# Kernel tuning notes

Hardware: AMD Instinct MI355X
Metric: run time of the kernel (lower is better)

Reference implementation:

```python
import jax, jax.numpy as jnp
import numpy as np

B, T = 32, 256
DM, DL, DH, DP, E = 256, 256, 512, 16, 8


def setup_inputs() -> dict:
    key = jax.random.key(0)
    ks = jax.random.split(key, 20)
    s = 0.02
    d = {
        "z": jax.random.normal(ks[0], (B, T, DL), jnp.float32),
        "p_next": jax.random.normal(ks[1], (B, T, DP), jnp.float32),
        "v_hip_next": jax.random.normal(ks[2], (B, T, 3), jnp.float32),
        "x_curr": jax.random.normal(ks[3], (B, T, DM), jnp.float32),
        # gating: Linear(DL+DP->DH), Linear(DL+DH->DH), Linear(DL+DH->E)
        "gw0": jax.random.normal(ks[4], (DL + DP, DH), jnp.float32) * s,
        "gb0": jnp.zeros((DH,), jnp.float32),
        "gw1": jax.random.normal(ks[5], (DL + DH, DH), jnp.float32) * s,
        "gb1": jnp.zeros((DH,), jnp.float32),
        "gw2": jax.random.normal(ks[6], (DL + DH, E), jnp.float32) * s,
        "gb2": jnp.zeros((E,), jnp.float32),
        # expert (MultiLinear) weights: (E, d_in, d_out)
        "w0": jax.random.normal(ks[7], (E, DM + 3 + DL, DH), jnp.float32) * s,
        "b0": jnp.zeros((E, DH), jnp.float32),
        "w1": jax.random.normal(ks[8], (E, DH + DL, DH), jnp.float32) * s,
        "b1": jnp.zeros((E, DH), jnp.float32),
        "w2": jax.random.normal(ks[9], (E, DH + DL, DH), jnp.float32) * s,
        "b2": jnp.zeros((E, DH), jnp.float32),
        "wo": jax.random.normal(ks[10], (E, DH + DL, DM), jnp.float32) * s,
        "bo": jnp.zeros((E, DM), jnp.float32),
    }
    return d


def _gating(z, p, gw0, gb0, gw1, gb1, gw2, gb2):
    h = jax.nn.elu(jnp.concatenate([z, p], axis=-1) @ gw0 + gb0)
    h = jax.nn.elu(jnp.concatenate([z, h], axis=-1) @ gw1 + gb1)
    h = jax.nn.softmax(jnp.concatenate([z, h], axis=-1) @ gw2 + gb2, axis=-1)
    return h  # (B, T, E)


def _moe_layer(x, w, b, ew):
    # x: (B,T,Din), w: (E,Din,Dout), b: (E,Dout), ew: (B,T,E)
    y = jnp.einsum('btd,edh->bteh', x, w) + b  # (B,T,E,Dout)
    return jnp.sum(y * ew[..., None], axis=-2)  # (B,T,Dout)


def reference(z, p_next, v_hip_next, x_curr,
              gw0, gb0, gw1, gb1, gw2, gb2,
              w0, b0, w1, b1, w2, b2, wo, bo):
    ew = _gating(z, p_next, gw0, gb0, gw1, gb1, gw2, gb2)
    x = jnp.concatenate([v_hip_next, x_curr], axis=-1)
    for w, b in ((w0, b0), (w1, b1), (w2, b2)):
        x = jnp.concatenate([z, x], axis=-1)
        x = jax.nn.elu(_moe_layer(x, w, b, ew))
    x = jnp.concatenate([z, x], axis=-1)
    return _moe_layer(x, wo, bo, ew)  # (B,T,DM)
```

## Files before the change

kernel.cpp:

```cpp
#include <hip/hip_runtime.h>
#include <cstdint>
#include <cstddef>

using u16 = unsigned short;
using bf16x8 = __attribute__((ext_vector_type(8))) __bf16;
using f32x4  = __attribute__((ext_vector_type(4))) float;

static __device__ __forceinline__ u16 f2bf(float f) {
  unsigned u = __builtin_bit_cast(unsigned, f);
  unsigned r = (u + 0x7fffu + ((u >> 16) & 1u)) >> 16;
  return (u16)r;
}
static __device__ __forceinline__ float bf2f(u16 h) {
  unsigned u = ((unsigned)h) << 16;
  return __builtin_bit_cast(float, u);
}
static __device__ __forceinline__ float eluf(float x) {
  return x > 0.f ? x : expm1f(x);
}
static __device__ __forceinline__ void gload16(const u16* g, u16* l) {
  __builtin_amdgcn_global_load_lds(
      (const __attribute__((address_space(1))) void*)g,
      (__attribute__((address_space(3))) void*)l, 16, 0, 0);
}

__global__ void transpose_convert(const float* __restrict__ src, u16* __restrict__ dst,
                                  int Ksrc, int Nsrc, int Kpad, int E) {
  __shared__ float tile[32][33];
  const int e  = blockIdx.z;
  const int k0 = blockIdx.x * 32;
  const int d0 = blockIdx.y * 32;
  const int tx = threadIdx.x;
  const int ty = threadIdx.y;
  const float* s = src + (size_t)e * Ksrc * Nsrc;
#pragma unroll
  for (int i = 0; i < 4; ++i) {
    const int k = k0 + ty + i * 8;
    float v = 0.f;
    if (k < Ksrc) v = s[(size_t)k * Nsrc + d0 + tx];
    tile[ty + i * 8][tx] = v;
  }
  __syncthreads();
#pragma unroll
  for (int i = 0; i < 4; ++i) {
    const int d = d0 + ty + i * 8;
    dst[((size_t)d * E + e) * Kpad + k0 + tx] = f2bf(tile[tx][ty + i * 8]);
  }
}

__global__ void prep_cat(const float* __restrict__ z, const float* __restrict__ p,
                         const float* __restrict__ vh, const float* __restrict__ xc,
                         u16* __restrict__ catP, u16* __restrict__ catE0,
                         u16* __restrict__ cat0, u16* __restrict__ cat1) {
  const int m = blockIdx.x;
  const int t = threadIdx.x;
  const u16 zb = f2bf(z[(size_t)m * 256 + t]);
  catP [(size_t)m * 288 + t] = zb;
  catE0[(size_t)m * 576 + t] = zb;
  cat0 [(size_t)m * 768 + t] = zb;
  cat1 [(size_t)m * 768 + t] = zb;
  if (t < 32) {
    const u16 val = (t < 16) ? f2bf(p[(size_t)m * 16 + t]) : (u16)0;
    catP[(size_t)m * 288 + 256 + t] = val;
  }
  for (int c = 256 + t; c < 576; c += 256) {
    const int idx = c - 256;
    float v = 0.f;
    if (idx < 3)        v = vh[(size_t)m * 3 + idx];
    else if (idx < 259) v = xc[(size_t)m * 256 + (idx - 3)];
    catE0[(size_t)m * 576 + c] = f2bf(v);
  }
}

__global__ __launch_bounds__(256) void gating_tail(const u16* __restrict__ cat,
                                                   const float* __restrict__ gw2,
                                                   const float* __restrict__ gb2,
                                                   float* __restrict__ ew) {
  const int ln = threadIdx.x & 63;
  const int token = (int)((blockIdx.x * 256 + threadIdx.x) >> 6);
  const u16* row = cat + (size_t)token * 768;
  float a[8] = {0.f, 0.f, 0.f, 0.f, 0.f, 0.f, 0.f, 0.f};
#pragma unroll
  for (int kk = 0; kk < 12; ++kk) {
    const int k = kk * 64 + ln;
    const float x = bf2f(row[k]);
    const float4* wr = reinterpret_cast<const float4*>(gw2 + (size_t)k * 8);
    const float4 w0 = wr[0], w1 = wr[1];
    a[0] += x * w0.x; a[1] += x * w0.y; a[2] += x * w0.z; a[3] += x * w0.w;
    a[4] += x * w1.x; a[5] += x * w1.y; a[6] += x * w1.z; a[7] += x * w1.w;
  }
#pragma unroll
  for (int j = 0; j < 8; ++j) {
#pragma unroll
    for (int d = 32; d > 0; d >>= 1) a[j] += __shfl_xor(a[j], d);
    a[j] += gb2[j];
  }
  float mx = a[0];
#pragma unroll
  for (int j = 1; j < 8; ++j) mx = fmaxf(mx, a[j]);
  float s = 0.f, pj[8];
#pragma unroll
  for (int j = 0; j < 8; ++j) { pj[j] = expf(a[j] - mx); s += pj[j]; }
  const float inv = 1.f / s;
  if (ln == 0) {
#pragma unroll
    for (int j = 0; j < 8; ++j) ew[(size_t)token * 8 + j] = pj[j] * inv;
  }
}

template <int MODE, int BK>
__global__ __launch_bounds__(256) void gemm_mfma(
    const u16* __restrict__ A, const u16* __restrict__ Bt,
    const float* __restrict__ bias, const float* __restrict__ ew,
    void* __restrict__ outp, int M, int N, int K,
    int out_stride, int out_col0) {
  constexpr int SLOTS = BK / 8;
  constexpr int SSH   = (BK == 32) ? 2 : 3;
  constexpr int CROWS = 1024 / (BK * 2);
  constexpr int LOADS = BK / 16;

  __shared__ alignas(16) u16 As[128 * BK];
  __shared__ alignas(16) u16 Bs[128 * BK];

  const int tid = threadIdx.x;
  const int ln  = tid & 63;
  const int wv  = tid >> 6;
  const int wr  = wv >> 1;
  const int wc  = wv & 1;
  const int m0  = blockIdx.y * 128;
  const int n0  = blockIdx.x * 128;

  const int lrow  = ln >> SSH;
  const int lslot = ln & (SLOTS - 1);
  const int fw    = (BK == 64) ? (lrow & 7) : ((lrow >> 1) & 3);
  const int gcol  = ((lslot ^ fw) << 3);
  const int c0    = wv * LOADS;

  const u16* gA[LOADS]; const u16* gB[LOADS];
  u16* lA[LOADS]; u16* lB[LOADS];
#pragma unroll
  for (int t = 0; t < LOADS; ++t) {
    const int rowg = (c0 + t) * CROWS + lrow;
    gA[t] = A  + (size_t)(m0 + rowg) * K + gcol;
    gB[t] = Bt + (size_t)(n0 + rowg) * K + gcol;
    lA[t] = &As[(size_t)(c0 + t) * 512];
    lB[t] = &Bs[(size_t)(c0 + t) * 512];
  }

  f32x4 acc[4][4];
#pragma unroll
  for (int i = 0; i < 4; ++i)
#pragma unroll
    for (int j = 0; j < 4; ++j) acc[i][j] = (f32x4){0.f, 0.f, 0.f, 0.f};

  const int ar  = ln & 15;
  const int hi  = ln >> 4;
  const int arf = (BK == 64) ? (ar & 7) : ((ar >> 1) & 3);

  const int kIters = K / BK;
  for (int kt = 0; kt < kIters; ++kt) {
#pragma unroll
    for (int t = 0; t < LOADS; ++t) gload16(gA[t], lA[t]);
#pragma unroll
    for (int t = 0; t < LOADS; ++t) gload16(gB[t], lB[t]);
#pragma unroll
    for (int t = 0; t < LOADS; ++t) { gA[t] += BK; gB[t] += BK; }
    __syncthreads();

#pragma unroll
    for (int k32 = 0; k32 < BK / 32; ++k32) {
      bf16x8 af[4], bfv[4];
#pragma unroll
      for (int i = 0; i < 4; ++i)
        af[i] = *reinterpret_cast<const bf16x8*>(
            &As[(size_t)(wr * 64 + i * 16 + ar) * BK + (((k32 * 4 + hi) ^ arf) << 3)]);
#pragma unroll
      for (int j = 0; j < 4; ++j)
        bfv[j] = *reinterpret_cast<const bf16x8*>(
            &Bs[(size_t)(wc * 64 + j * 16 + ar) * BK + (((k32 * 4 + hi) ^ arf) << 3)]);
#pragma unroll
      for (int i = 0; i < 4; ++i)
#pragma unroll
        for (int j = 0; j < 4; ++j)
          acc[i][j] = __builtin_amdgcn_mfma_f32_16x16x32_bf16(af[i], bfv[j], acc[i][j], 0, 0, 0);
    }
    __syncthreads();
  }

  const int m0w = m0 + wr * 64 + (ln >> 4) * 4;
  const int n0w = n0 + wc * 64 + (ln & 15);
  u16* outb = (u16*)outp;
#pragma unroll
  for (int j = 0; j < 4; ++j) {
    const int n = n0w + j * 16;
    const float bv = bias[n];
#pragma unroll
    for (int i = 0; i < 4; ++i) {
#pragma unroll
      for (int r = 0; r < 4; ++r) {
        const int m = m0w + i * 16 + r;
        outb[(size_t)m * out_stride + out_col0 + n] = f2bf(eluf(acc[i][j][r] + bv));
      }
    }
  }
}

template <int MODE>
__global__ __launch_bounds__(256, 3) void gemm128e(
    const u16* __restrict__ A, const u16* __restrict__ Bt,
    const float* __restrict__ bias, const float* __restrict__ ew,
    void* __restrict__ outp, int N, int K, int out_stride, int out_col0) {
  constexpr int BK = 64;
  __shared__ alignas(16) u16 As[128 * BK];
  __shared__ alignas(16) u16 Bs[128 * BK];

  const int tid = threadIdx.x;
  const int ln  = tid & 63;
  const int wv  = tid >> 6;
  const int wr  = wv >> 1;
  const int wc  = wv & 1;
  const int m0  = blockIdx.y * 128;
  const int n0  = blockIdx.x * 128;

  const int lrow  = ln >> 3;
  const int gslot = (ln & 7) ^ lrow;
  const u16* gA[4]; const u16* gB[4];
#pragma unroll
  for (int q = 0; q < 4; ++q) {
    const int row = wv * 32 + q * 8 + lrow;
    gA[q] = A  + (size_t)(m0 + row) * K + gslot * 8;
    gB[q] = Bt + (size_t)(n0 + row) * K + gslot * 8;
  }

  f32x4 acc[4][4];
#pragma unroll
  for (int i = 0; i < 4; ++i)
#pragma unroll
    for (int j = 0; j < 4; ++j) acc[i][j] = (f32x4){0.f, 0.f, 0.f, 0.f};

  const int ar  = ln & 15;
  const int hi  = ln >> 4;
  const int arf = ar & 7;
  const int sl0 = (hi ^ arf) << 3;
  const int sl1 = ((4 + hi) ^ arf) << 3;

  const int nt = K / BK;

  for (int t = 0; t < nt; ++t) {
#pragma unroll
    for (int q = 0; q < 4; ++q) {
      gload16(gA[q], &As[(size_t)(wv * 32 + q * 8) * 64]);
      gload16(gB[q], &Bs[(size_t)(wv * 32 + q * 8) * 64]);
      gA[q] += BK; gB[q] += BK;
    }
    __syncthreads();

    const u16* Ab = &As[(size_t)(wr * 64 + ar) * BK];
    const u16* Bb = &Bs[(size_t)(wc * 64 + ar) * BK];
#pragma unroll
    for (int kk = 0; kk < 2; ++kk) {
      const int sl = kk ? sl1 : sl0;
      bf16x8 av[4], bv[4];
#pragma unroll
      for (int i = 0; i < 4; ++i)
        av[i] = *reinterpret_cast<const bf16x8*>(Ab + (size_t)i * 16 * BK + sl);
#pragma unroll
      for (int j = 0; j < 4; ++j)
        bv[j] = *reinterpret_cast<const bf16x8*>(Bb + (size_t)j * 16 * BK + sl);
      __builtin_amdgcn_s_setprio(1);
#pragma unroll
      for (int i = 0; i < 4; ++i)
#pragma unroll
        for (int j = 0; j < 4; ++j)
          acc[i][j] = __builtin_amdgcn_mfma_f32_16x16x32_bf16(bv[i], av[j], acc[i][j], 0, 0, 0);
      __builtin_amdgcn_s_setprio(0);
    }
    __syncthreads();
  }

  const int lm = ln & 15;
  const int e0 = (hi & 1) * 4;
  const int dhalf = hi >> 1;
  const int Dout = N >> 3;

  float ewv[4][4];
#pragma unroll
  for (int j = 0; j < 4; ++j) {
    const int m = m0 + wr * 64 + j * 16 + lm;
#pragma unroll
    for (int r = 0; r < 4; ++r) ewv[j][r] = ew[(size_t)m * 8 + e0 + r];
  }
  float bs[4][4];
#pragma unroll
  for (int i = 0; i < 4; ++i) {
    const int di = ((n0 + wc * 64 + i * 16) >> 3) + dhalf;
#pragma unroll
    for (int r = 0; r < 4; ++r) bs[i][r] = bias[(size_t)(e0 + r) * Dout + di];
  }

#pragma unroll
  for (int i = 0; i < 4; ++i) {
    const int di = ((n0 + wc * 64 + i * 16) >> 3) + dhalf;
#pragma unroll
    for (int j = 0; j < 4; ++j) {
      float s = 0.f;
#pragma unroll
      for (int r = 0; r < 4; ++r)
        s += (acc[i][j][r] + bs[i][r]) * ewv[j][r];
      s += __shfl_xor(s, 16);
      if ((hi & 1) == 0) {
        const int m = m0 + wr * 64 + j * 16 + lm;
        if (MODE == 1) {
          ((u16*)outp)[(size_t)m * out_stride + out_col0 + di] = f2bf(eluf(s));
        } else {
          ((float*)outp)[(size_t)m * out_stride + di] = s;
        }
      }
    }
  }
}

extern "C" void kernel_launch(void* const* d_in, const int* in_sizes, int n_in,
                              void* d_out, int out_size, void* d_ws, size_t ws_size,
                              hipStream_t stream) {
  const float* z   = (const float*)d_in[0];
  const float* p   = (const float*)d_in[1];
  const float* vh  = (const float*)d_in[2];
  const float* xc  = (const float*)d_in[3];
  const float* gw0 = (const float*)d_in[4];
  const float* gb0 = (const float*)d_in[5];
  const float* gw1 = (const float*)d_in[6];
  const float* gb1 = (const float*)d_in[7];
  const float* gw2 = (const float*)d_in[8];
  const float* gb2 = (const float*)d_in[9];
  const float* w0  = (const float*)d_in[10];
  const float* b0  = (const float*)d_in[11];
  const float* w1  = (const float*)d_in[12];
  const float* b1  = (const float*)d_in[13];
  const float* w2  = (const float*)d_in[14];
  const float* b2  = (const float*)d_in[15];
  const float* wo  = (const float*)d_in[16];
  const float* bo  = (const float*)d_in[17];
  float* out = (float*)d_out;

  char* ws = (char*)d_ws;
  size_t off = 0;
  auto alloc = [&](size_t bytes) {
    char* pp = ws + off;
    off += (bytes + 255) & ~(size_t)255;
    return pp;
  };
  u16* gw0t  = (u16*)alloc((size_t)512 * 288 * 2);
  u16* gw1t  = (u16*)alloc((size_t)512 * 768 * 2);
  u16* w0t   = (u16*)alloc((size_t)4096 * 576 * 2);
  u16* w1t   = (u16*)alloc((size_t)4096 * 768 * 2);
  u16* w2t   = (u16*)alloc((size_t)4096 * 768 * 2);
  u16* wot   = (u16*)alloc((size_t)2048 * 768 * 2);
  u16* catP  = (u16*)alloc((size_t)8192 * 288 * 2);
  u16* catE0 = (u16*)alloc((size_t)8192 * 576 * 2);
  u16* cat0  = (u16*)alloc((size_t)8192 * 768 * 2);
  u16* cat1  = (u16*)alloc((size_t)8192 * 768 * 2);
  float* ew  = (float*)alloc((size_t)8192 * 8 * 4);
  (void)ws_size; (void)in_sizes; (void)n_in; (void)out_size;

  const dim3 tb(32, 8);
  transpose_convert<<<dim3(9, 16, 1),  tb, 0, stream>>>(gw0, gw0t, 272, 512, 288, 1);
  transpose_convert<<<dim3(24, 16, 1), tb, 0, stream>>>(gw1, gw1t, 768, 512, 768, 1);
  transpose_convert<<<dim3(18, 16, 8), tb, 0, stream>>>(w0,  w0t,  515, 512, 576, 8);
  transpose_convert<<<dim3(24, 16, 8), tb, 0, stream>>>(w1,  w1t,  768, 512, 768, 8);
  transpose_convert<<<dim3(24, 16, 8), tb, 0, stream>>>(w2,  w2t,  768, 512, 768, 8);
  transpose_convert<<<dim3(24, 8, 8),  tb, 0, stream>>>(wo,  wot,  768, 256, 768, 8);
  prep_cat<<<8192, 256, 0, stream>>>(z, p, vh, xc, catP, catE0, cat0, cat1);

  gemm_mfma<0, 32><<<dim3(4, 64), 256, 0, stream>>>(catP, gw0t, gb0, nullptr, cat0,
                                                    8192, 512, 288, 768, 256);
  gemm_mfma<0, 64><<<dim3(4, 64), 256, 0, stream>>>(cat0, gw1t, gb1, nullptr, cat1,
                                                    8192, 512, 768, 768, 256);
  gating_tail<<<2048, 256, 0, stream>>>(cat1, gw2, gb2, ew);

  gemm128e<1><<<dim3(32, 64), 256, 0, stream>>>(catE0, w0t, b0, ew, cat0,
                                                4096, 576, 768, 256);
  gemm128e<1><<<dim3(32, 64), 256, 0, stream>>>(cat0, w1t, b1, ew, cat1,
                                                4096, 768, 768, 256);
  gemm128e<1><<<dim3(32, 64), 256, 0, stream>>>(cat1, w2t, b2, ew, cat0,
                                                4096, 768, 768, 256);
  gemm128e<2><<<dim3(16, 64), 256, 0, stream>>>(cat0, wot, bo, ew, out,
                                                2048, 768, 256, 0);
}
```

Measured before the change: 291.3 us.

## Use 32x32 MFMA in expert GEMM, merge transposes, add 64-row gating GEMM

The expert GEMM inner loop moves from 16x16x32 to 32x32x16 bf16 MFMA tiles, and the mixture epilogue is reworked to match the new accumulator layout. This cuts LDS fragment reads per MFMA. The six weight-transpose launches are merged into one kernel that dispatches on block id, to remove launch overhead. The second gating GEMM gets a new kernel with a 64x128 tile, which doubles the block count to fill more CUs. The 32x32 accumulators raise register pressure under the existing launch bounds of 3 blocks per SM.

```diff
diff --git a/kernel.cpp b/kernel.cpp
--- a/kernel.cpp
+++ b/kernel.cpp
@@ -5,6 +5,7 @@
 using u16 = unsigned short;
 using bf16x8 = __attribute__((ext_vector_type(8))) __bf16;
 using f32x4  = __attribute__((ext_vector_type(4))) float;
+using f32x16 = __attribute__((ext_vector_type(16))) float;
 
 static __device__ __forceinline__ u16 f2bf(float f) {
   unsigned u = __builtin_bit_cast(unsigned, f);
@@ -24,12 +25,30 @@
       (__attribute__((address_space(3))) void*)l, 16, 0, 0);
 }
 
-__global__ void transpose_convert(const float* __restrict__ src, u16* __restrict__ dst,
-                                  int Ksrc, int Nsrc, int Kpad, int E) {
+__global__ void transpose_all(const float* __restrict__ s0, u16* __restrict__ d0,
+                              const float* __restrict__ s1, u16* __restrict__ d1,
+                              const float* __restrict__ s2, u16* __restrict__ d2,
+                              const float* __restrict__ s3, u16* __restrict__ d3,
+                              const float* __restrict__ s4, u16* __restrict__ d4,
+                              const float* __restrict__ s5, u16* __restrict__ d5) {
+  const int bid = blockIdx.x;
+  const float* src; u16* dst;
+  int Ksrc, Nsrc, Kpad, nKb, local;
+  if (bid < 144)       { src=s0; dst=d0; Ksrc=272; Nsrc=512; Kpad=288; nKb=9;  local=bid; }
+  else if (bid < 528)  { src=s1; dst=d1; Ksrc=768; Nsrc=512; Kpad=768; nKb=24; local=bid-144; }
+  else if (bid < 2832) { src=s2; dst=d2; Ksrc=515; Nsrc=512; Kpad=576; nKb=18; local=bid-528; }
+  else if (bid < 5904) { src=s3; dst=d3; Ksrc=768; Nsrc=512; Kpad=768; nKb=24; local=bid-2832; }
+  else if (bid < 8976) { src=s4; dst=d4; Ksrc=768; Nsrc=512; Kpad=768; nKb=24; local=bid-5904; }
+  else                 { src=s5; dst=d5; Ksrc=768; Nsrc=256; Kpad=768; nKb=24; local=bid-8976; }
+  const int nDb   = Nsrc >> 5;
+  const int perE  = nKb * nDb;
+  const int e     = local / perE;
+  const int rem   = local - e * perE;
+  const int k0    = (rem % nKb) * 32;
+  const int d0i   = (rem / nKb) * 32;
+  const int E     = (bid < 528) ? 1 : 8;
+
   __shared__ float tile[32][33];
-  const int e  = blockIdx.z;
-  const int k0 = blockIdx.x * 32;
-  const int d0 = blockIdx.y * 32;
   const int tx = threadIdx.x;
   const int ty = threadIdx.y;
   const float* s = src + (size_t)e * Ksrc * Nsrc;
@@ -37,13 +56,13 @@
   for (int i = 0; i < 4; ++i) {
     const int k = k0 + ty + i * 8;
     float v = 0.f;
-    if (k < Ksrc) v = s[(size_t)k * Nsrc + d0 + tx];
+    if (k < Ksrc) v = s[(size_t)k * Nsrc + d0i + tx];
     tile[ty + i * 8][tx] = v;
   }
   __syncthreads();
 #pragma unroll
   for (int i = 0; i < 4; ++i) {
-    const int d = d0 + ty + i * 8;
+    const int d = d0i + ty + i * 8;
     dst[((size_t)d * E + e) * Kpad + k0 + tx] = f2bf(tile[tx][ty + i * 8]);
   }
 }
@@ -205,6 +224,95 @@
   }
 }
 
+__global__ __launch_bounds__(256) void gemm_g(
+    const u16* __restrict__ A, const u16* __restrict__ Bt,
+    const float* __restrict__ bias, void* __restrict__ outp,
+    int K, int out_stride, int out_col0) {
+  constexpr int BK = 64;
+  __shared__ alignas(16) u16 As[64 * BK];
+  __shared__ alignas(16) u16 Bs[128 * BK];
+
+  const int tid = threadIdx.x;
+  const int ln  = tid & 63;
+  const int wv  = tid >> 6;
+  const int wc  = wv;
+  const int m0  = blockIdx.y * 64;
+  const int n0  = blockIdx.x * 128;
+
+  const int lrow  = ln >> 3;
+  const int gslot = (ln & 7) ^ lrow;
+  const u16* gA[2]; const u16* gB[4];
+#pragma unroll
+  for (int q = 0; q < 2; ++q)
+    gA[q] = A + (size_t)(m0 + (wv * 2 + q) * 8 + lrow) * K + gslot * 8;
+#pragma unroll
+  for (int q = 0; q < 4; ++q)
+    gB[q] = Bt + (size_t)(n0 + (wv * 4 + q) * 8 + lrow) * K + gslot * 8;
+
+  f32x4 acc[4][2];
+#pragma unroll
+  for (int i = 0; i < 4; ++i)
+#pragma unroll
+    for (int j = 0; j < 2; ++j) acc[i][j] = (f32x4){0.f, 0.f, 0.f, 0.f};
+
+  const int ar  = ln & 15;
+  const int hi  = ln >> 4;
+  const int arf = ar & 7;
+  const int sl0 = (hi ^ arf) << 3;
+  const int sl1 = ((4 + hi) ^ arf) << 3;
+
+  const int nt = K / BK;
+  for (int t = 0; t < nt; ++t) {
+#pragma unroll
+    for (int q = 0; q < 2; ++q) {
+      gload16(gA[q], &As[(size_t)((wv * 2 + q) * 8) * 64]);
+      gA[q] += BK;
+    }
+#pragma unroll
+    for (int q = 0; q < 4; ++q) {
+      gload16(gB[q], &Bs[(size_t)((wv * 4 + q) * 8) * 64]);
+      gB[q] += BK;
+    }
+    __syncthreads();
+
+#pragma unroll
+    for (int kk = 0; kk < 2; ++kk) {
+      const int sl = kk ? sl1 : sl0;
+      bf16x8 av[4], bv[2];
+#pragma unroll
+      for (int i = 0; i < 4; ++i)
+        av[i] = *reinterpret_cast<const bf16x8*>(&As[(size_t)(i * 16 + ar) * 64 + sl]);
+#pragma unroll
+      for (int j = 0; j < 2; ++j)
+        bv[j] = *reinterpret_cast<const bf16x8*>(
+            &Bs[(size_t)(wc * 32 + j * 16 + ar) * 64 + sl]);
+      __builtin_amdgcn_s_setprio(1);
+#pragma unroll
+      for (int i = 0; i < 4; ++i)
+#pragma unroll
+        for (int j = 0; j < 2; ++j)
+          acc[i][j] = __builtin_amdgcn_mfma_f32_16x16x32_bf16(av[i], bv[j], acc[i][j], 0, 0, 0);
+      __builtin_amdgcn_s_setprio(0);
+    }
+    __syncthreads();
+  }
+
+  u16* outb = (u16*)outp;
+#pragma unroll
+  for (int j = 0; j < 2; ++j) {
+    const int n = n0 + wc * 32 + j * 16 + (ln & 15);
+    const float bv = bias[n];
+#pragma unroll
+    for (int i = 0; i < 4; ++i) {
+#pragma unroll
+      for (int r = 0; r < 4; ++r) {
+        const int m = m0 + i * 16 + hi * 4 + r;
+        outb[(size_t)m * out_stride + out_col0 + n] = f2bf(eluf(acc[i][j][r] + bv));
+      }
+    }
+  }
+}
+
 template <int MODE>
 __global__ __launch_bounds__(256, 3) void gemm128e(
     const u16* __restrict__ A, const u16* __restrict__ Bt,
@@ -232,17 +340,17 @@
     gB[q] = Bt + (size_t)(n0 + row) * K + gslot * 8;
   }
 
-  f32x4 acc[4][4];
-#pragma unroll
-  for (int i = 0; i < 4; ++i)
-#pragma unroll
-    for (int j = 0; j < 4; ++j) acc[i][j] = (f32x4){0.f, 0.f, 0.f, 0.f};
-
-  const int ar  = ln & 15;
-  const int hi  = ln >> 4;
-  const int arf = ar & 7;
-  const int sl0 = (hi ^ arf) << 3;
-  const int sl1 = ((4 + hi) ^ arf) << 3;
+  f32x16 acc[2][2];
+#pragma unroll
+  for (int i = 0; i < 2; ++i)
+#pragma unroll
+    for (int j = 0; j < 2; ++j)
+#pragma unroll
+      for (int r = 0; r < 16; ++r) acc[i][j][r] = 0.f;
+
+  const int ar32 = ln & 31;
+  const int hi2  = ln >> 5;
+  const int arf  = ar32 & 7;
 
   const int nt = K / BK;
 
@@ -255,65 +363,67 @@
     }
     __syncthreads();
 
-    const u16* Ab = &As[(size_t)(wr * 64 + ar) * BK];
-    const u16* Bb = &Bs[(size_t)(wc * 64 + ar) * BK];
-#pragma unroll
-    for (int kk = 0; kk < 2; ++kk) {
-      const int sl = kk ? sl1 : sl0;
-      bf16x8 av[4], bv[4];
-#pragma unroll
-      for (int i = 0; i < 4; ++i)
-        av[i] = *reinterpret_cast<const bf16x8*>(Ab + (size_t)i * 16 * BK + sl);
-#pragma unroll
-      for (int j = 0; j < 4; ++j)
-        bv[j] = *reinterpret_cast<const bf16x8*>(Bb + (size_t)j * 16 * BK + sl);
-      __builtin_amdgcn_s_setprio(1);
-#pragma unroll
-      for (int i = 0; i < 4; ++i)
-#pragma unroll
-        for (int j = 0; j < 4; ++j)
-          acc[i][j] = __builtin_amdgcn_mfma_f32_16x16x32_bf16(bv[i], av[j], acc[i][j], 0, 0, 0);
-      __builtin_amdgcn_s_setprio(0);
-    }
-    __syncthreads();
-  }
-
-  const int lm = ln & 15;
-  const int e0 = (hi & 1) * 4;
-  const int dhalf = hi >> 1;
+    const u16* Ab = &As[(size_t)(wr * 64 + ar32) * 64];
+    const u16* Bb = &Bs[(size_t)(wc * 64 + ar32) * 64];
+    __builtin_amdgcn_s_setprio(1);
+#pragma unroll
+    for (int kk = 0; kk < 4; ++kk) {
+      const int sl = (((kk * 2 + hi2) ^ arf) << 3);
+      bf16x8 bv[2], av[2];
+#pragma unroll
+      for (int f = 0; f < 2; ++f) {
+        bv[f] = *reinterpret_cast<const bf16x8*>(Bb + (size_t)f * 32 * 64 + sl);
+        av[f] = *reinterpret_cast<const bf16x8*>(Ab + (size_t)f * 32 * 64 + sl);
+      }
+#pragma unroll
+      for (int i = 0; i < 2; ++i)
+#pragma unroll
+        for (int j = 0; j < 2; ++j)
+          acc[i][j] = __builtin_amdgcn_mfma_f32_32x32x16_bf16(bv[i], av[j], acc[i][j], 0, 0, 0);
+    }
+    __builtin_amdgcn_s_setprio(0);
+    __syncthreads();
+  }
+
   const int Dout = N >> 3;
-
-  float ewv[4][4];
-#pragma unroll
-  for (int j = 0; j < 4; ++j) {
-    const int m = m0 + wr * 64 + j * 16 + lm;
-#pragma unroll
-    for (int r = 0; r < 4; ++r) ewv[j][r] = ew[(size_t)m * 8 + e0 + r];
-  }
-  float bs[4][4];
-#pragma unroll
-  for (int i = 0; i < 4; ++i) {
-    const int di = ((n0 + wc * 64 + i * 16) >> 3) + dhalf;
-#pragma unroll
-    for (int r = 0; r < 4; ++r) bs[i][r] = bias[(size_t)(e0 + r) * Dout + di];
-  }
-
-#pragma unroll
-  for (int i = 0; i < 4; ++i) {
-    const int di = ((n0 + wc * 64 + i * 16) >> 3) + dhalf;
-#pragma unroll
-    for (int j = 0; j < 4; ++j) {
-      float s = 0.f;
+  float ewv[2][4];
+#pragma unroll
+  for (int j = 0; j < 2; ++j) {
+    const int m = m0 + wr * 64 + j * 32 + ar32;
+#pragma unroll
+    for (int r = 0; r < 4; ++r) ewv[j][r] = ew[(size_t)m * 8 + r + 4 * hi2];
+  }
+  float bs[2][4][4];
+#pragma unroll
+  for (int i = 0; i < 2; ++i) {
+    const int nb = (n0 + wc * 64 + i * 32) >> 3;
+#pragma unroll
+    for (int dq = 0; dq < 4; ++dq)
 #pragma unroll
       for (int r = 0; r < 4; ++r)
-        s += (acc[i][j][r] + bs[i][r]) * ewv[j][r];
-      s += __shfl_xor(s, 16);
-      if ((hi & 1) == 0) {
-        const int m = m0 + wr * 64 + j * 16 + lm;
-        if (MODE == 1) {
-          ((u16*)outp)[(size_t)m * out_stride + out_col0 + di] = f2bf(eluf(s));
-        } else {
-          ((float*)outp)[(size_t)m * out_stride + di] = s;
+        bs[i][dq][r] = bias[(size_t)(r + 4 * hi2) * Dout + nb + dq];
+  }
+
+#pragma unroll
+  for (int i = 0; i < 2; ++i) {
+    const int nb = (n0 + wc * 64 + i * 32) >> 3;
+#pragma unroll
+    for (int j = 0; j < 2; ++j) {
+      const int m = m0 + wr * 64 + j * 32 + ar32;
+#pragma unroll
+      for (int dq = 0; dq < 4; ++dq) {
+        float s = 0.f;
+#pragma unroll
+        for (int r = 0; r < 4; ++r)
+          s += (acc[i][j][dq * 4 + r] + bs[i][dq][r]) * ewv[j][r];
+        s += __shfl_xor(s, 32);
+        if (hi2 == 0) {
+          const int d = nb + dq;
+          if (MODE == 1) {
+            ((u16*)outp)[(size_t)m * out_stride + out_col0 + d] = f2bf(eluf(s));
+          } else {
+            ((float*)outp)[(size_t)m * out_stride + d] = s;
+          }
         }
       }
     }
@@ -363,19 +473,14 @@
   float* ew  = (float*)alloc((size_t)8192 * 8 * 4);
   (void)ws_size; (void)in_sizes; (void)n_in; (void)out_size;
 
-  const dim3 tb(32, 8);
-  transpose_convert<<<dim3(9, 16, 1),  tb, 0, stream>>>(gw0, gw0t, 272, 512, 288, 1);
-  transpose_convert<<<dim3(24, 16, 1), tb, 0, stream>>>(gw1, gw1t, 768, 512, 768, 1);
-  transpose_convert<<<dim3(18, 16, 8), tb, 0, stream>>>(w0,  w0t,  515, 512, 576, 8);
-  transpose_convert<<<dim3(24, 16, 8), tb, 0, stream>>>(w1,  w1t,  768, 512, 768, 8);
-  transpose_convert<<<dim3(24, 16, 8), tb, 0, stream>>>(w2,  w2t,  768, 512, 768, 8);
-  transpose_convert<<<dim3(24, 8, 8),  tb, 0, stream>>>(wo,  wot,  768, 256, 768, 8);
+  transpose_all<<<10512, dim3(32, 8), 0, stream>>>(gw0, gw0t, gw1, gw1t,
+                                                   w0, w0t, w1, w1t,
+                                                   w2, w2t, wo, wot);
   prep_cat<<<8192, 256, 0, stream>>>(z, p, vh, xc, catP, catE0, cat0, cat1);
 
   gemm_mfma<0, 32><<<dim3(4, 64), 256, 0, stream>>>(catP, gw0t, gb0, nullptr, cat0,
                                                     8192, 512, 288, 768, 256);
-  gemm_mfma<0, 64><<<dim3(4, 64), 256, 0, stream>>>(cat0, gw1t, gb1, nullptr, cat1,
-                                                    8192, 512, 768, 768, 256);
+  gemm_g<<<dim3(4, 128), 256, 0, stream>>>(cat0, gw1t, gb1, cat1, 768, 768, 256);
   gating_tail<<<2048, 256, 0, stream>>>(cat1, gw2, gb2, ew);
 
   gemm128e<1><<<dim3(32, 64), 256, 0, stream>>>(catE0, w0t, b0, ew, cat0,
```

Result: slower. 300.1 us (+3.0%).
